# Kernel optimization log

Hardware: AMD Instinct MI355X
Metric: run time of the kernel (lower is better)

## Reference

```python
import jax, jax.numpy as jnp
import numpy as np

NH, NOPE_D, ROPE_D, V_D, R = 16, 48, 16, 64, 128
EPS = 1e-6

def rms_norm(x, w):
    norm = jax.lax.rsqrt(jnp.mean(jnp.square(x), axis=-1, keepdims=True) + EPS)
    return x * norm * w

def apply_rope(x, cos, sin):
    # x: (..., rope_d); cos/sin broadcastable (..., rope_d//2)
    d = x.shape[-1]
    x1, x2 = x[..., : d // 2], x[..., d // 2 :]
    return jnp.concatenate([x1 * cos - x2 * sin, x2 * cos + x1 * sin], axis=-1)

def setup_inputs() -> dict:
    key = jax.random.key(0)
    ks = jax.random.split(key, 8)
    B, T, D = 2, 2048, 1024
    s = lambda fan_in: 1.0 / np.sqrt(fan_in)
    return {
        "x": jax.random.normal(ks[0], (B, T, D), jnp.float32),
        "cos": jax.random.uniform(ks[1], (T, ROPE_D // 2), jnp.float32),
        "sin": jax.random.uniform(ks[2], (T, ROPE_D // 2), jnp.float32),
        "Wq": jax.random.normal(ks[3], (NH * (NOPE_D + ROPE_D), D), jnp.float32) * s(D),
        "q_norm_w": jnp.ones((NOPE_D + ROPE_D,), jnp.float32),
        "Wkva": jax.random.normal(ks[4], (R + ROPE_D, D), jnp.float32) * s(D),
        "kva_norm_w": jnp.ones((R,), jnp.float32),
        "Wkvb": jax.random.normal(ks[5], (NH * (NOPE_D + V_D), R), jnp.float32) * s(R),
        "Wo": jax.random.normal(ks[6], (D, NH * V_D), jnp.float32) * s(NH * V_D),
    }

def reference(x, cos, sin, Wq, q_norm_w, Wkva, kva_norm_w, Wkvb, Wo):
    B, T, D = x.shape
    # Q path: project, per-head RMSNorm over (nope+rope) dims, split
    q = (x @ Wq.T).reshape(B, T, NH, NOPE_D + ROPE_D)
    q = rms_norm(q, q_norm_w)
    q_nope, q_rope = q[..., :NOPE_D], q[..., NOPE_D:]
    # Low-rank KV path
    kv_a = x @ Wkva.T  # (B,T,R+ROPE_D)
    kv_latent = rms_norm(kv_a[..., :R], kva_norm_w)
    k_rope_raw = kv_a[..., R:]  # (B,T,ROPE_D) shared across heads
    kv_b = (kv_latent @ Wkvb.T).reshape(B, T, NH, NOPE_D + V_D)
    k_nope, v = kv_b[..., :NOPE_D], kv_b[..., NOPE_D:]
    # Decoupled RoPE
    cos_t = cos[None, :T, None, :]  # (1,T,1,rope_d/2)
    sin_t = sin[None, :T, None, :]
    q_rope = apply_rope(q_rope, cos_t, sin_t)
    k_rope = apply_rope(k_rope_raw[:, :, None, :], cos[None, :T, None, :], sin[None, :T, None, :])
    k_rope = jnp.broadcast_to(k_rope, (B, T, NH, ROPE_D))
    q_full = jnp.concatenate([q_nope, q_rope], axis=-1)  # (B,T,NH,64)
    k_full = jnp.concatenate([k_nope, k_rope], axis=-1)
    # Causal attention, scale = 1/sqrt(nope+rope)
    scale = (NOPE_D + ROPE_D) ** -0.5
    scores = jnp.einsum("bqhd,bkhd->bhqk", q_full, k_full) * scale
    causal = jnp.tril(jnp.ones((T, T), bool))
    scores = jnp.where(causal[None, None], scores, -jnp.inf)
    attn = jax.nn.softmax(scores, axis=-1)
    out = jnp.einsum("bhqk,bkhd->bqhd", attn, v).reshape(B, T, NH * V_D)
    return out @ Wo.T
```

## Files before the change

kernel.cpp:

```cpp
#include <hip/hip_runtime.h>
#include <hip/hip_bf16.h>
#include <math.h>

#define NH 16
#define T_ 2048
#define B_ 2
#define D_ 1024
#define EPS 1e-6f

typedef __attribute__((ext_vector_type(8))) short bf16x8;
typedef __attribute__((ext_vector_type(4))) short bf16x4;
typedef __attribute__((ext_vector_type(4))) float f32x4;

__device__ __forceinline__ unsigned pack_bf16(float a, float b){
  __hip_bfloat162 t = __float22bfloat162_rn(make_float2(a, b));
  unsigned r; __builtin_memcpy(&r, &t, 4); return r;
}

__device__ __forceinline__ void gload_lds16(const void* g, void* l){
  __builtin_amdgcn_global_load_lds((const __attribute__((address_space(1))) void*)g,
                                   (__attribute__((address_space(3))) void*)l, 16, 0, 0);
}

__device__ __forceinline__ f32x4 mfma16(bf16x4 a, bf16x4 b, f32x4 c){
#if __has_builtin(__builtin_amdgcn_mfma_f32_16x16x16bf16_1k)
  return __builtin_amdgcn_mfma_f32_16x16x16bf16_1k(a, b, c, 0, 0, 0);
#else
  asm volatile("v_mfma_f32_16x16x16_bf16 %0, %1, %2, %0" : "+v"(c) : "v"(a), "v"(b));
  return c;
#endif
}

__global__ __launch_bounds__(256)
void cvt5(const float* __restrict__ x, const float* __restrict__ wq,
          const float* __restrict__ wkva, const float* __restrict__ wkvb,
          const float* __restrict__ wo,
          __hip_bfloat16* __restrict__ xb, __hip_bfloat16* __restrict__ wqb,
          __hip_bfloat16* __restrict__ wkvab, __hip_bfloat16* __restrict__ wkvbb,
          __hip_bfloat16* __restrict__ wob)
{
  const int i = blockIdx.x * 256 + threadIdx.x;
  const float* s; __hip_bfloat16* d; size_t soff, doff;
  if      (i < 1048576) { s = x;    d = xb;    soff = doff = i; }
  else if (i < 1310720) { s = wq;   d = wqb;   soff = doff = i - 1048576; }
  else if (i < 1347584) { s = wkva; d = wkvab; soff = doff = i - 1310720; }
  else if (i < 1404928) {
    const int off = i - 1347584;
    const int srow = off >> 5, c4 = off & 31;
    const int h = srow / 112, dd = srow % 112;
    const int drow = (dd < 48) ? (h*48 + dd) : (768 + h*64 + (dd - 48));
    s = wkvb; d = wkvbb; soff = off; doff = (size_t)drow*32 + c4;
  }
  else                  { s = wo;   d = wob;   soff = doff = i - 1404928; }
  float4 v = *(const float4*)(s + soff * 4);
  *(__hip_bfloat162*)(d + doff * 4)     = __float22bfloat162_rn(make_float2(v.x, v.y));
  *(__hip_bfloat162*)(d + doff * 4 + 2) = __float22bfloat162_rn(make_float2(v.z, v.w));
}

template<typename CT>
__global__ __launch_bounds__(256, 2)
void gemm_bt64(const __hip_bfloat16* __restrict__ A, const __hip_bfloat16* __restrict__ W,
               CT* __restrict__ C, int M, int N, int K)
{
  __shared__ __hip_bfloat16 As[2][128 * 64];
  __shared__ __hip_bfloat16 Ws[2][64 * 64];
  const int tid = threadIdx.x;
  const int wv = tid >> 6, lane = tid & 63;
  const int m = lane & 15, quad = lane >> 4;
  const int bm = blockIdx.y * 128, bn = blockIdx.x * 64;

  const __hip_bfloat16* ga[4];
  const __hip_bfloat16* gw[2];
  #pragma unroll
  for (int i = 0; i < 4; i++) {
    const int slot = i*256 + tid;
    const int row = slot >> 3, cb = slot & 7;
    ga[i] = A + (size_t)(bm + row) * K + ((cb ^ (row & 7)) << 3);
  }
  #pragma unroll
  for (int i = 0; i < 2; i++) {
    const int slot = i*256 + tid;
    const int row = slot >> 3, cb = slot & 7;
    int wr = bn + row; if (wr >= N) wr = N - 1;
    gw[i] = W + (size_t)wr * K + ((cb ^ (row & 7)) << 3);
  }
  auto stage = [&](int buf){
    #pragma unroll
    for (int i = 0; i < 4; i++) { gload_lds16(ga[i], &As[buf][(i*256 + wv*64)*8]); ga[i] += 64; }
    #pragma unroll
    for (int i = 0; i < 2; i++) { gload_lds16(gw[i], &Ws[buf][(i*256 + wv*64)*8]); gw[i] += 64; }
  };

  f32x4 acc[2][4];
  #pragma unroll
  for (int mi = 0; mi < 2; mi++)
    #pragma unroll
    for (int nj = 0; nj < 4; nj++) acc[mi][nj] = (f32x4){0.f,0.f,0.f,0.f};

  stage(0);
  const int iters = K >> 6;
  for (int it = 0; it < iters; it++) {
    const int cur = it & 1;
    __syncthreads();
    if (it + 1 < iters) stage(cur ^ 1);
    #pragma unroll
    for (int ks = 0; ks < 2; ks++) {
      const int cb = ((ks*4 + quad) ^ (m & 7)) << 3;
      bf16x8 af[2], wf[4];
      #pragma unroll
      for (int mi = 0; mi < 2; mi++)
        af[mi] = *(const bf16x8*)(&As[cur][(wv*32 + mi*16 + m) * 64 + cb]);
      #pragma unroll
      for (int nj = 0; nj < 4; nj++)
        wf[nj] = *(const bf16x8*)(&Ws[cur][(nj*16 + m) * 64 + cb]);
      #pragma unroll
      for (int mi = 0; mi < 2; mi++)
        #pragma unroll
        for (int nj = 0; nj < 4; nj++)
          acc[mi][nj] = __builtin_amdgcn_mfma_f32_16x16x32_bf16(af[mi], wf[nj], acc[mi][nj], 0, 0, 0);
    }
  }

  #pragma unroll
  for (int mi = 0; mi < 2; mi++)
    #pragma unroll
    for (int nj = 0; nj < 4; nj++) {
      const int col = bn + nj*16 + m;
      if (col < N) {
        #pragma unroll
        for (int r = 0; r < 4; r++) {
          const int row = bm + wv*32 + mi*16 + quad*4 + r;
          if constexpr (sizeof(CT) == 2)
            C[(size_t)row * N + col] = (CT)__float2bfloat16(acc[mi][nj][r]);
          else
            C[(size_t)row * N + col] = acc[mi][nj][r];
        }
      }
    }
}

__global__ __launch_bounds__(256, 2)
void gemm_qkva(const __hip_bfloat16* __restrict__ A, const __hip_bfloat16* __restrict__ Wqb,
               const __hip_bfloat16* __restrict__ Wkvab,
               const float* __restrict__ qw, const float* __restrict__ kw,
               const float* __restrict__ cosp, const float* __restrict__ sinp,
               __hip_bfloat16* __restrict__ qb, __hip_bfloat16* __restrict__ kvl16,
               __hip_bfloat16* __restrict__ krope16)
{
  __shared__ __hip_bfloat16 As[2][128 * 64];
  __shared__ __hip_bfloat16 Ws[2][128 * 64];
  const int K = 1024;
  const int tid = threadIdx.x;
  const int wv = tid >> 6, lane = tid & 63;
  const int m = lane & 15, quad = lane >> 4;
  const int wr = wv >> 1, wc = wv & 1;
  const int bm = blockIdx.y * 128;
  const bool isq = blockIdx.x < 8;
  const __hip_bfloat16* W = isq ? Wqb : Wkvab;
  const int bn = isq ? blockIdx.x*128 : (blockIdx.x - 8)*128;
  const int Nw = isq ? 1024 : 144;

  const __hip_bfloat16* ga[4];
  const __hip_bfloat16* gw[4];
  #pragma unroll
  for (int i = 0; i < 4; i++) {
    const int slot = i*256 + tid;
    const int row = slot >> 3, cb = slot & 7;
    ga[i] = A + (size_t)(bm + row) * K + ((cb ^ (row & 7)) << 3);
    int wrow = bn + row; if (wrow >= Nw) wrow = Nw - 1;
    gw[i] = W + (size_t)wrow * K + ((cb ^ (row & 7)) << 3);
  }
  auto stage = [&](int buf){
    #pragma unroll
    for (int i = 0; i < 4; i++) { gload_lds16(ga[i], &As[buf][(i*256 + wv*64)*8]); ga[i] += 64; }
    #pragma unroll
    for (int i = 0; i < 4; i++) { gload_lds16(gw[i], &Ws[buf][(i*256 + wv*64)*8]); gw[i] += 64; }
  };

  f32x4 acc[4][4];
  #pragma unroll
  for (int mi = 0; mi < 4; mi++)
    #pragma unroll
    for (int nj = 0; nj < 4; nj++) acc[mi][nj] = (f32x4){0.f,0.f,0.f,0.f};

  stage(0);
  for (int it = 0; it < 16; it++) {
    const int cur = it & 1;
    __syncthreads();
    if (it < 15) stage(cur ^ 1);
    #pragma unroll
    for (int ks = 0; ks < 2; ks++) {
      const int cb = ((ks*4 + quad) ^ (m & 7)) << 3;
      bf16x8 af[4], wf[4];
      #pragma unroll
      for (int mi = 0; mi < 4; mi++)
        af[mi] = *(const bf16x8*)(&As[cur][(wr*64 + mi*16 + m) * 64 + cb]);
      #pragma unroll
      for (int nj = 0; nj < 4; nj++)
        wf[nj] = *(const bf16x8*)(&Ws[cur][(wc*64 + nj*16 + m) * 64 + cb]);
      #pragma unroll
      for (int mi = 0; mi < 4; mi++)
        #pragma unroll
        for (int nj = 0; nj < 4; nj++)
          acc[mi][nj] = __builtin_amdgcn_mfma_f32_16x16x32_bf16(af[mi], wf[nj], acc[mi][nj], 0, 0, 0);
    }
  }

  if (isq) {
    const int head = blockIdx.x*2 + wc;
    float qwv[4];
    #pragma unroll
    for (int nj = 0; nj < 4; nj++) qwv[nj] = qw[nj*16 + m];
    const int j = m & 7;
    const float qscale = 0.125f * 1.44269504f;
    #pragma unroll
    for (int mi = 0; mi < 4; mi++) {
      #pragma unroll
      for (int r = 0; r < 4; r++) {
        float ss = 0.f;
        #pragma unroll
        for (int nj = 0; nj < 4; nj++) { const float t = acc[mi][nj][r]; ss = fmaf(t, t, ss); }
        ss += __shfl_xor(ss, 1, 64); ss += __shfl_xor(ss, 2, 64);
        ss += __shfl_xor(ss, 4, 64); ss += __shfl_xor(ss, 8, 64);
        const float nrm = rsqrtf(ss * (1.0f/64.0f) + EPS);
        float v[4];
        #pragma unroll
        for (int nj = 0; nj < 4; nj++) v[nj] = acc[mi][nj][r] * nrm * qwv[nj];
        const int grow = bm + wr*64 + mi*16 + quad*4 + r;
        const int t = grow & (T_ - 1);
        const int b = grow >> 11;
        const float part = __shfl_xor(v[3], 8, 64);
        const float c = cosp[t*8 + j], sn = sinp[t*8 + j];
        v[3] = (m < 8) ? (v[3]*c - part*sn) : (v[3]*c + part*sn);
        __hip_bfloat16* dst = qb + ((size_t)(b*NH + head)*T_ + t)*64 + m;
        #pragma unroll
        for (int nj = 0; nj < 4; nj++) dst[nj*16] = __float2bfloat16(v[nj] * qscale);
      }
    }
  } else if (bn == 0) {
    __syncthreads();
    float* P = (float*)As;
    float part[4][4];
    #pragma unroll
    for (int mi = 0; mi < 4; mi++)
      #pragma unroll
      for (int r = 0; r < 4; r++) {
        float ss = 0.f;
        #pragma unroll
        for (int nj = 0; nj < 4; nj++) { const float t = acc[mi][nj][r]; ss = fmaf(t, t, ss); }
        ss += __shfl_xor(ss, 1, 64); ss += __shfl_xor(ss, 2, 64);
        ss += __shfl_xor(ss, 4, 64); ss += __shfl_xor(ss, 8, 64);
        part[mi][r] = ss;
        if (m == 0) P[((wc*2 + wr)*4 + mi)*16 + quad*4 + r] = ss;
      }
    __syncthreads();
    float kwv[4];
    #pragma unroll
    for (int nj = 0; nj < 4; nj++) kwv[nj] = kw[wc*64 + nj*16 + m];
    #pragma unroll
    for (int mi = 0; mi < 4; mi++)
      #pragma unroll
      for (int r = 0; r < 4; r++) {
        const float tot = part[mi][r] + P[(((wc^1)*2 + wr)*4 + mi)*16 + quad*4 + r];
        const float nrm = rsqrtf(tot * (1.0f/128.0f) + EPS);
        const int row = bm + wr*64 + mi*16 + quad*4 + r;
        #pragma unroll
        for (int nj = 0; nj < 4; nj++)
          kvl16[(size_t)row*128 + wc*64 + nj*16 + m]
              = __float2bfloat16(acc[mi][nj][r] * nrm * kwv[nj]);
      }
  } else {
    if (wc == 0) {
      const int j = m & 7;
      #pragma unroll
      for (int mi = 0; mi < 4; mi++)
        #pragma unroll
        for (int r = 0; r < 4; r++) {
          const int row = bm + wr*64 + mi*16 + quad*4 + r;
          const int t = row & (T_ - 1);
          const float v = acc[mi][0][r];
          const float part = __shfl_xor(v, 8, 64);
          const float c = cosp[t*8 + j], sn = sinp[t*8 + j];
          krope16[(size_t)row*16 + m] = __float2bfloat16((m < 8) ? (v*c - part*sn)
                                                                 : (v*c + part*sn));
        }
    }
  }
}

__global__ __launch_bounds__(256, 2)
void gemm_kvb(const __hip_bfloat16* __restrict__ A, const __hip_bfloat16* __restrict__ W,
              __hip_bfloat16* __restrict__ knope, __hip_bfloat16* __restrict__ vt)
{
  __shared__ __hip_bfloat16 As[2][128 * 64];
  __shared__ __hip_bfloat16 Ws[2][64 * 64];
  const int K = 128;
  const int tid = threadIdx.x;
  const int wv = tid >> 6, lane = tid & 63;
  const int m = lane & 15, quad = lane >> 4;
  const int bm = blockIdx.y * 128, bn = blockIdx.x * 64;

  const __hip_bfloat16* ga[4];
  const __hip_bfloat16* gw[2];
  #pragma unroll
  for (int i = 0; i < 4; i++) {
    const int slot = i*256 + tid;
    const int row = slot >> 3, cb = slot & 7;
    ga[i] = A + (size_t)(bm + row) * K + ((cb ^ (row & 7)) << 3);
  }
  #pragma unroll
  for (int i = 0; i < 2; i++) {
    const int slot = i*256 + tid;
    const int row = slot >> 3, cb = slot & 7;
    gw[i] = W + (size_t)(bn + row) * K + ((cb ^ (row & 7)) << 3);
  }
  auto stage = [&](int buf){
    #pragma unroll
    for (int i = 0; i < 4; i++) { gload_lds16(ga[i], &As[buf][(i*256 + wv*64)*8]); ga[i] += 64; }
    #pragma unroll
    for (int i = 0; i < 2; i++) { gload_lds16(gw[i], &Ws[buf][(i*256 + wv*64)*8]); gw[i] += 64; }
  };

  f32x4 acc[2][4];
  #pragma unroll
  for (int mi = 0; mi < 2; mi++)
    #pragma unroll
    for (int nj = 0; nj < 4; nj++) acc[mi][nj] = (f32x4){0.f,0.f,0.f,0.f};

  stage(0);
  for (int it = 0; it < 2; it++) {
    const int cur = it & 1;
    __syncthreads();
    if (it == 0) stage(1);
    #pragma unroll
    for (int ks = 0; ks < 2; ks++) {
      const int cb = ((ks*4 + quad) ^ (m & 7)) << 3;
      bf16x8 af[2], wf[4];
      #pragma unroll
      for (int mi = 0; mi < 2; mi++)
        af[mi] = *(const bf16x8*)(&As[cur][(wv*32 + mi*16 + m) * 64 + cb]);
      #pragma unroll
      for (int nj = 0; nj < 4; nj++)
        wf[nj] = *(const bf16x8*)(&Ws[cur][(nj*16 + m) * 64 + cb]);
      #pragma unroll
      for (int mi = 0; mi < 2; mi++)
        #pragma unroll
        for (int nj = 0; nj < 4; nj++)
          acc[mi][nj] = __builtin_amdgcn_mfma_f32_16x16x32_bf16(af[mi], wf[nj], acc[mi][nj], 0, 0, 0);
    }
  }

  if (bn < 768) {
    #pragma unroll
    for (int mi = 0; mi < 2; mi++)
      #pragma unroll
      for (int nj = 0; nj < 4; nj++) {
        const int col = bn + nj*16 + m;
        #pragma unroll
        for (int r = 0; r < 4; r++) {
          const int row = bm + wv*32 + mi*16 + quad*4 + r;
          knope[(size_t)row * 768 + col] = __float2bfloat16(acc[mi][nj][r]);
        }
      }
  } else {
    __syncthreads();
    short* TL = (short*)&As[0][0];
    #pragma unroll
    for (int mi = 0; mi < 2; mi++)
      #pragma unroll
      for (int nj = 0; nj < 4; nj++) {
        const int d = nj*16 + m;
        #pragma unroll
        for (int r = 0; r < 4; r++) {
          const int tl = wv*32 + mi*16 + quad*4 + r;
          __hip_bfloat16 hv = __float2bfloat16(acc[mi][nj][r]);
          short sv; __builtin_memcpy(&sv, &hv, 2);
          TL[d*136 + tl] = sv;
        }
      }
    __syncthreads();
    const int h = (bn - 768) >> 6;
    const int b = bm >> 11;
    const int t0 = bm & (T_ - 1);
    #pragma unroll
    for (int i = 0; i < 4; i++) {
      const int unit = i*256 + tid;
      const int d = unit >> 4, tu = unit & 15;
      *(bf16x8*)(vt + ((size_t)(b*NH + h)*64 + d)*T_ + t0 + tu*8)
          = *(const bf16x8*)(TL + d*136 + tu*8);
    }
  }
}

__global__ __launch_bounds__(256, 4)
void attn_tile(const __hip_bfloat16* __restrict__ qb,
               const __hip_bfloat16* __restrict__ knope,
               const __hip_bfloat16* __restrict__ krope16,
               const __hip_bfloat16* __restrict__ vt16,
               __hip_bfloat16* __restrict__ aout)
{
  __shared__ __hip_bfloat16 SL[16384];
  const int tid = threadIdx.x;
  const int wv = tid >> 6, lane = tid & 63;
  const int m = lane & 15, quad = lane >> 4;
  const int wq = wv >> 1, wk = wv & 1;
  const int idx = (blockIdx.x + blockIdx.y) & 31;
  const int pj = idx & 7, pk = idx >> 3;
  const int qt = (pk == 0) ? pj : (pk == 1) ? (15 - pj) : (pk == 2) ? (16 + pj) : (31 - pj);
  const int bh = blockIdx.y;
  const int b = bh >> 4, h = bh & 15;
  const int nt = qt + 1;

  bf16x8 q0[2], q1[2];
  #pragma unroll
  for (int t2 = 0; t2 < 2; t2++) {
    const __hip_bfloat16* qr = qb + ((size_t)bh*T_ + qt*64 + wq*32 + t2*16 + m)*64 + quad*8;
    q0[t2] = *(const bf16x8*)qr; q1[t2] = *(const bf16x8*)(qr + 32);
  }

  const __hip_bfloat16* pK[2]; size_t iK[2];
  const __hip_bfloat16* pV[2];
  #pragma unroll
  for (int i = 0; i < 2; i++) {
    const int slot = i*256 + tid;
    const int krow = slot >> 3;
    const int kde = (slot & 7) ^ (krow & 7);
    if (kde < 6) { pK[i] = knope + (size_t)(b*T_ + krow)*768 + h*48 + kde*8; iK[i] = (size_t)64*768; }
    else         { pK[i] = krope16 + (size_t)(b*T_ + krow)*16 + (kde-6)*8;   iK[i] = (size_t)64*16; }
    pV[i] = vt16 + ((size_t)bh*64 + krow)*T_ + kde*8;
  }

  auto stage = [&](int buf){
    #pragma unroll
    for (int i = 0; i < 2; i++) {
      gload_lds16(pK[i], SL + buf*4096 + (i*256 + wv*64)*8);
      gload_lds16(pV[i], SL + 8192 + buf*4096 + (i*256 + wv*64)*8);
      pK[i] += iK[i]; pV[i] += 64;
    }
  };

  f32x4 o[2][4];
  #pragma unroll
  for (int t2 = 0; t2 < 2; t2++)
    #pragma unroll
    for (int vs = 0; vs < 4; vs++) o[t2][vs] = (f32x4){0.f,0.f,0.f,0.f};
  float lrun[2] = {0.f, 0.f};

  const int swk = quad ^ (m & 7);
  const int qh = quad >> 1, ql = quad & 1;
  stage(0);

  for (int kt = 0; kt < nt; kt++) {
    const int cur = kt & 1;
    __syncthreads();
    if (kt + 1 < nt) stage(cur ^ 1);
    const __hip_bfloat16* Kc = SL + cur*4096;
    const __hip_bfloat16* Vc = SL + 8192 + cur*4096;
    const bool dtile = (kt == qt);

    f32x4 s[2][2];
    __builtin_amdgcn_s_setprio(1);
    #pragma unroll
    for (int ks = 0; ks < 2; ks++) {
      const int gk2 = 2*wk + ks;
      if (!dtile || gk2 <= 2*wq + 1) {
        const __hip_bfloat16* kr = Kc + (wk*32 + ks*16 + m)*64;
        const bf16x8 kf0 = *(const bf16x8*)(kr + swk*8);
        const bf16x8 kf1 = *(const bf16x8*)(kr + (swk^4)*8);
        #pragma unroll
        for (int t2 = 0; t2 < 2; t2++) {
          if (!dtile || gk2 <= 2*wq + t2) {
            f32x4 z = (f32x4){0.f,0.f,0.f,0.f};
            z = __builtin_amdgcn_mfma_f32_16x16x32_bf16(kf0, q0[t2], z, 0, 0, 0);
            z = __builtin_amdgcn_mfma_f32_16x16x32_bf16(kf1, q1[t2], z, 0, 0, 0);
            s[t2][ks] = z;
          } else {
            s[t2][ks] = (f32x4){-1e30f,-1e30f,-1e30f,-1e30f};
          }
        }
      } else {
        s[0][ks] = (f32x4){-1e30f,-1e30f,-1e30f,-1e30f};
        s[1][ks] = (f32x4){-1e30f,-1e30f,-1e30f,-1e30f};
      }
    }
    __builtin_amdgcn_s_setprio(0);

    if (dtile) {
      #pragma unroll
      for (int ks = 0; ks < 2; ks++)
        #pragma unroll
        for (int t2 = 0; t2 < 2; t2++)
          if (2*wk + ks == 2*wq + t2) {
            #pragma unroll
            for (int r = 0; r < 4; r++)
              if (quad*4 + r > m) s[t2][ks][r] = -1e30f;
          }
    }

    bf16x4 u[2][2];
    #pragma unroll
    for (int t2 = 0; t2 < 2; t2++)
      #pragma unroll
      for (int ks = 0; ks < 2; ks++) {
        float p0 = exp2f(s[t2][ks][0] - 48.0f), p1 = exp2f(s[t2][ks][1] - 48.0f);
        float p2 = exp2f(s[t2][ks][2] - 48.0f), p3 = exp2f(s[t2][ks][3] - 48.0f);
        lrun[t2] += (p0 + p1) + (p2 + p3);
        union { unsigned ui[2]; bf16x4 v; } uu;
        uu.ui[0] = pack_bf16(p0, p1);
        uu.ui[1] = pack_bf16(p2, p3);
        u[t2][ks] = uu.v;
      }

    __builtin_amdgcn_s_setprio(1);
    #pragma unroll
    for (int vs = 0; vs < 4; vs++) {
      #pragma unroll
      for (int ks = 0; ks < 2; ks++) {
        const int gk2 = 2*wk + ks;
        if (!dtile || gk2 <= 2*wq + 1) {
          const bf16x4 vf = *(const bf16x4*)(Vc + (vs*16 + m)*64
                              + (((wk*4 + ks*2 + qh) ^ (m & 7)) << 3) + (ql << 2));
          #pragma unroll
          for (int t2 = 0; t2 < 2; t2++)
            if (!dtile || gk2 <= 2*wq + t2)
              o[t2][vs] = mfma16(vf, u[t2][ks], o[t2][vs]);
        }
      }
    }
    __builtin_amdgcn_s_setprio(0);
  }

  __syncthreads();
  float* FB = (float*)SL;
  float* LB = ((float*)SL) + 4096;
  if (wk == 1) {
    #pragma unroll
    for (int t2 = 0; t2 < 2; t2++)
      #pragma unroll
      for (int vs = 0; vs < 4; vs++)
        #pragma unroll
        for (int r = 0; r < 4; r++)
          FB[wq*2048 + ((t2*4 + vs)*4 + r)*64 + lane] = o[t2][vs][r];
    LB[wq*128 + lane]      = lrun[0];
    LB[wq*128 + 64 + lane] = lrun[1];
  }
  __syncthreads();
  if (wk == 0) {
    #pragma unroll
    for (int t2 = 0; t2 < 2; t2++)
      #pragma unroll
      for (int vs = 0; vs < 4; vs++)
        #pragma unroll
        for (int r = 0; r < 4; r++)
          o[t2][vs][r] += FB[wq*2048 + ((t2*4 + vs)*4 + r)*64 + lane];
    lrun[0] += LB[wq*128 + lane];
    lrun[1] += LB[wq*128 + 64 + lane];
    #pragma unroll
    for (int t2 = 0; t2 < 2; t2++) {
      float l = lrun[t2];
      l += __shfl_xor(l, 16, 64);
      l += __shfl_xor(l, 32, 64);
      const float inv = 1.0f / l;
      const size_t base = (size_t)(b*T_ + qt*64 + wq*32 + t2*16 + m) * 1024 + h*64 + quad*4;
      #pragma unroll
      for (int vs = 0; vs < 4; vs++) {
        union { unsigned ui[2]; bf16x4 v; } pkv;
        pkv.ui[0] = pack_bf16(o[t2][vs][0] * inv, o[t2][vs][1] * inv);
        pkv.ui[1] = pack_bf16(o[t2][vs][2] * inv, o[t2][vs][3] * inv);
        *(bf16x4*)(aout + base + vs*16) = pkv.v;
      }
    }
  }
}

extern "C" void kernel_launch(void* const* d_in, const int* in_sizes, int n_in,
                              void* d_out, int out_size, void* d_ws, size_t ws_size,
                              hipStream_t stream)
{
  const float* x    = (const float*)d_in[0];
  const float* cosp = (const float*)d_in[1];
  const float* sinp = (const float*)d_in[2];
  const float* Wq   = (const float*)d_in[3];
  const float* qw   = (const float*)d_in[4];
  const float* Wkva = (const float*)d_in[5];
  const float* kw   = (const float*)d_in[6];
  const float* Wkvb = (const float*)d_in[7];
  const float* Wo   = (const float*)d_in[8];
  float* out = (float*)d_out;

  float* kva = (float*)d_ws;
  __hip_bfloat16* xb16    = (__hip_bfloat16*)(kva + 589824);
  __hip_bfloat16* knope16 = xb16 + 4194304;
  __hip_bfloat16* kvl16   = knope16 + 3145728;
  __hip_bfloat16* qb16    = kvl16 + 524288;
  __hip_bfloat16* vt16    = qb16 + 4194304;
  __hip_bfloat16* krope16 = vt16 + 4194304;
  __hip_bfloat16* Wqb     = krope16 + 65536;
  __hip_bfloat16* Wkvab   = Wqb + 1048576;
  __hip_bfloat16* Wkvbb   = Wkvab + 147456;
  __hip_bfloat16* Wob     = Wkvbb + 229376;
  __hip_bfloat16* ab16    = Wob + 1048576;

  const int M = B_ * T_;

  cvt5<<<6512, 256, 0, stream>>>(x, Wq, Wkva, Wkvb, Wo, xb16, Wqb, Wkvab, Wkvbb, Wob);
  gemm_qkva<<<dim3(10, 32), 256, 0, stream>>>(xb16, Wqb, Wkvab, qw, kw, cosp, sinp,
                                              qb16, kvl16, krope16);
  gemm_kvb<<<dim3(28, 32), 256, 0, stream>>>(kvl16, Wkvbb, knope16, vt16);
  attn_tile<<<dim3(32, B_ * NH), 256, 0, stream>>>(qb16, knope16, krope16, vt16, ab16);
  gemm_bt64<float><<<dim3(16, 32), 256, 0, stream>>>(ab16, Wob, out, M, 1024, 1024);
}
```

Before: 178.0 us.

## Split long causal query tiles across blocks and merge partials via atomic counter

Reassigns causal attention work so that each block handles a roughly equal number of key tiles. The longest query tiles (24-31) are split into two key-range halves run by different blocks. Each half writes unnormalised partial outputs and row sums to workspace scratch and bumps an atomic counter; the second block to finish merges both halves and writes the output. The counters are zeroed in the conversion kernel. This trades extra scratch traffic and a global atomic handshake for a shorter critical path than the previous uneven per-block tile counts.

```diff
diff --git a/kernel.cpp b/kernel.cpp
--- a/kernel.cpp
+++ b/kernel.cpp
@@ -37,8 +37,9 @@
           const float* __restrict__ wo,
           __hip_bfloat16* __restrict__ xb, __hip_bfloat16* __restrict__ wqb,
           __hip_bfloat16* __restrict__ wkvab, __hip_bfloat16* __restrict__ wkvbb,
-          __hip_bfloat16* __restrict__ wob)
+          __hip_bfloat16* __restrict__ wob, int* __restrict__ ctr)
 {
+  if (blockIdx.x == 0) ctr[threadIdx.x] = 0;
   const int i = blockIdx.x * 256 + threadIdx.x;
   const float* s; __hip_bfloat16* d; size_t soff, doff;
   if      (i < 1048576) { s = x;    d = xb;    soff = doff = i; }
@@ -397,177 +398,245 @@
                const __hip_bfloat16* __restrict__ knope,
                const __hip_bfloat16* __restrict__ krope16,
                const __hip_bfloat16* __restrict__ vt16,
-               __hip_bfloat16* __restrict__ aout)
+               __hip_bfloat16* __restrict__ aout,
+               float* __restrict__ scr, int* __restrict__ ctr)
 {
   __shared__ __hip_bfloat16 SL[16384];
+  __shared__ int flagv;
   const int tid = threadIdx.x;
   const int wv = tid >> 6, lane = tid & 63;
   const int m = lane & 15, quad = lane >> 4;
   const int wq = wv >> 1, wk = wv & 1;
-  const int idx = (blockIdx.x + blockIdx.y) & 31;
-  const int pj = idx & 7, pk = idx >> 3;
-  const int qt = (pk == 0) ? pj : (pk == 1) ? (15 - pj) : (pk == 2) ? (16 + pj) : (31 - pj);
   const int bh = blockIdx.y;
   const int b = bh >> 4, h = bh & 15;
-  const int nt = qt + 1;
-
-  bf16x8 q0[2], q1[2];
-  #pragma unroll
-  for (int t2 = 0; t2 < 2; t2++) {
-    const __hip_bfloat16* qr = qb + ((size_t)bh*T_ + qt*64 + wq*32 + t2*16 + m)*64 + quad*8;
-    q0[t2] = *(const bf16x8*)qr; q1[t2] = *(const bf16x8*)(qr + 32);
-  }
-
-  const __hip_bfloat16* pK[2]; size_t iK[2];
-  const __hip_bfloat16* pV[2];
-  #pragma unroll
-  for (int i = 0; i < 2; i++) {
-    const int slot = i*256 + tid;
-    const int krow = slot >> 3;
-    const int kde = (slot & 7) ^ (krow & 7);
-    if (kde < 6) { pK[i] = knope + (size_t)(b*T_ + krow)*768 + h*48 + kde*8; iK[i] = (size_t)64*768; }
-    else         { pK[i] = krope16 + (size_t)(b*T_ + krow)*16 + (kde-6)*8;   iK[i] = (size_t)64*16; }
-    pV[i] = vt16 + ((size_t)bh*64 + krow)*T_ + kde*8;
-  }
-
-  auto stage = [&](int buf){
-    #pragma unroll
-    for (int i = 0; i < 2; i++) {
-      gload_lds16(pK[i], SL + buf*4096 + (i*256 + wv*64)*8);
-      gload_lds16(pV[i], SL + 8192 + buf*4096 + (i*256 + wv*64)*8);
-      pK[i] += iK[i]; pV[i] += 64;
-    }
-  };
-
-  f32x4 o[2][4];
-  #pragma unroll
-  for (int t2 = 0; t2 < 2; t2++)
-    #pragma unroll
-    for (int vs = 0; vs < 4; vs++) o[t2][vs] = (f32x4){0.f,0.f,0.f,0.f};
-  float lrun[2] = {0.f, 0.f};
+
+  const int idx = (blockIdx.x + blockIdx.y) & 31;
+  const int i = idx & 7, p = idx >> 3;
+  int nseg = 1, sQt[2], sK0[2], sNk[2], sMd[2];
+  if (i < 7) {
+    if      (p == 0) { sQt[0]=23-i; sK0[0]=0;  sNk[0]=24-i; sMd[0]=0; }
+    else if (p == 1) { sQt[0]=24+i; sK0[0]=0;  sNk[0]=16;   sMd[0]=1; }
+    else if (p == 2) { sQt[0]=8+i;  sK0[0]=0;  sNk[0]=9+i;  sMd[0]=0; }
+    else { nseg=2; sQt[0]=i;    sK0[0]=0;  sNk[0]=i+1;  sMd[0]=0;
+                   sQt[1]=31-i; sK0[1]=16; sNk[1]=16-i; sMd[1]=2; }
+  } else {
+    if      (p == 0) { sQt[0]=15; sK0[0]=0;  sNk[0]=16; sMd[0]=0; }
+    else if (p == 1) { sQt[0]=16; sK0[0]=0;  sNk[0]=17; sMd[0]=0; }
+    else if (p == 2) { nseg=2; sQt[0]=7;  sK0[0]=0;  sNk[0]=8; sMd[0]=0;
+                               sQt[1]=24; sK0[1]=16; sNk[1]=9; sMd[1]=2; }
+    else             { sQt[0]=31; sK0[0]=0;  sNk[0]=16; sMd[0]=1; }
+  }
 
   const int swk = quad ^ (m & 7);
   const int qh = quad >> 1, ql = quad & 1;
-  stage(0);
-
-  for (int kt = 0; kt < nt; kt++) {
-    const int cur = kt & 1;
-    __syncthreads();
-    if (kt + 1 < nt) stage(cur ^ 1);
-    const __hip_bfloat16* Kc = SL + cur*4096;
-    const __hip_bfloat16* Vc = SL + 8192 + cur*4096;
-    const bool dtile = (kt == qt);
-
-    f32x4 s[2][2];
-    __builtin_amdgcn_s_setprio(1);
-    #pragma unroll
-    for (int ks = 0; ks < 2; ks++) {
-      const int gk2 = 2*wk + ks;
-      if (!dtile || gk2 <= 2*wq + 1) {
-        const __hip_bfloat16* kr = Kc + (wk*32 + ks*16 + m)*64;
-        const bf16x8 kf0 = *(const bf16x8*)(kr + swk*8);
-        const bf16x8 kf1 = *(const bf16x8*)(kr + (swk^4)*8);
-        #pragma unroll
-        for (int t2 = 0; t2 < 2; t2++) {
-          if (!dtile || gk2 <= 2*wq + t2) {
-            f32x4 z = (f32x4){0.f,0.f,0.f,0.f};
-            z = __builtin_amdgcn_mfma_f32_16x16x32_bf16(kf0, q0[t2], z, 0, 0, 0);
-            z = __builtin_amdgcn_mfma_f32_16x16x32_bf16(kf1, q1[t2], z, 0, 0, 0);
-            s[t2][ks] = z;
-          } else {
-            s[t2][ks] = (f32x4){-1e30f,-1e30f,-1e30f,-1e30f};
-          }
-        }
-      } else {
-        s[0][ks] = (f32x4){-1e30f,-1e30f,-1e30f,-1e30f};
-        s[1][ks] = (f32x4){-1e30f,-1e30f,-1e30f,-1e30f};
-      }
-    }
-    __builtin_amdgcn_s_setprio(0);
-
-    if (dtile) {
-      #pragma unroll
-      for (int ks = 0; ks < 2; ks++)
-        #pragma unroll
-        for (int t2 = 0; t2 < 2; t2++)
-          if (2*wk + ks == 2*wq + t2) {
-            #pragma unroll
-            for (int r = 0; r < 4; r++)
-              if (quad*4 + r > m) s[t2][ks][r] = -1e30f;
-          }
-    }
-
-    bf16x4 u[2][2];
+
+  for (int sg = 0; sg < nseg; sg++) {
+    const int qt = sQt[sg], k0 = sK0[sg], nk = sNk[sg], md = sMd[sg];
+
+    bf16x8 q0[2], q1[2];
+    #pragma unroll
+    for (int t2 = 0; t2 < 2; t2++) {
+      const __hip_bfloat16* qr = qb + ((size_t)bh*T_ + qt*64 + wq*32 + t2*16 + m)*64 + quad*8;
+      q0[t2] = *(const bf16x8*)qr; q1[t2] = *(const bf16x8*)(qr + 32);
+    }
+
+    const __hip_bfloat16* pK[2]; size_t iK[2];
+    const __hip_bfloat16* pV[2];
+    #pragma unroll
+    for (int ii = 0; ii < 2; ii++) {
+      const int slot = ii*256 + tid;
+      const int krow = slot >> 3;
+      const int kde = (slot & 7) ^ (krow & 7);
+      if (kde < 6) { pK[ii] = knope + (size_t)(b*T_ + k0*64 + krow)*768 + h*48 + kde*8; iK[ii] = (size_t)64*768; }
+      else         { pK[ii] = krope16 + (size_t)(b*T_ + k0*64 + krow)*16 + (kde-6)*8;   iK[ii] = (size_t)64*16; }
+      pV[ii] = vt16 + ((size_t)bh*64 + krow)*T_ + k0*64 + kde*8;
+    }
+    auto stage = [&](int buf){
+      #pragma unroll
+      for (int ii = 0; ii < 2; ii++) {
+        gload_lds16(pK[ii], SL + buf*4096 + (ii*256 + wv*64)*8);
+        gload_lds16(pV[ii], SL + 8192 + buf*4096 + (ii*256 + wv*64)*8);
+        pK[ii] += iK[ii]; pV[ii] += 64;
+      }
+    };
+
+    f32x4 o[2][4];
     #pragma unroll
     for (int t2 = 0; t2 < 2; t2++)
       #pragma unroll
-      for (int ks = 0; ks < 2; ks++) {
-        float p0 = exp2f(s[t2][ks][0] - 48.0f), p1 = exp2f(s[t2][ks][1] - 48.0f);
-        float p2 = exp2f(s[t2][ks][2] - 48.0f), p3 = exp2f(s[t2][ks][3] - 48.0f);
-        lrun[t2] += (p0 + p1) + (p2 + p3);
-        union { unsigned ui[2]; bf16x4 v; } uu;
-        uu.ui[0] = pack_bf16(p0, p1);
-        uu.ui[1] = pack_bf16(p2, p3);
-        u[t2][ks] = uu.v;
-      }
-
-    __builtin_amdgcn_s_setprio(1);
-    #pragma unroll
-    for (int vs = 0; vs < 4; vs++) {
+      for (int vs = 0; vs < 4; vs++) o[t2][vs] = (f32x4){0.f,0.f,0.f,0.f};
+    float lrun[2] = {0.f, 0.f};
+
+    __syncthreads();
+    stage(0);
+
+    for (int k2 = 0; k2 < nk; k2++) {
+      const int kt = k0 + k2;
+      const int cur = k2 & 1;
+      __syncthreads();
+      if (k2 + 1 < nk) stage(cur ^ 1);
+      const __hip_bfloat16* Kc = SL + cur*4096;
+      const __hip_bfloat16* Vc = SL + 8192 + cur*4096;
+      const bool dtile = (kt == qt);
+
+      f32x4 s[2][2];
+      __builtin_amdgcn_s_setprio(1);
       #pragma unroll
       for (int ks = 0; ks < 2; ks++) {
         const int gk2 = 2*wk + ks;
         if (!dtile || gk2 <= 2*wq + 1) {
-          const bf16x4 vf = *(const bf16x4*)(Vc + (vs*16 + m)*64
-                              + (((wk*4 + ks*2 + qh) ^ (m & 7)) << 3) + (ql << 2));
+          const __hip_bfloat16* kr = Kc + (wk*32 + ks*16 + m)*64;
+          const bf16x8 kf0 = *(const bf16x8*)(kr + swk*8);
+          const bf16x8 kf1 = *(const bf16x8*)(kr + (swk^4)*8);
+          #pragma unroll
+          for (int t2 = 0; t2 < 2; t2++) {
+            if (!dtile || gk2 <= 2*wq + t2) {
+              f32x4 z = (f32x4){0.f,0.f,0.f,0.f};
+              z = __builtin_amdgcn_mfma_f32_16x16x32_bf16(kf0, q0[t2], z, 0, 0, 0);
+              z = __builtin_amdgcn_mfma_f32_16x16x32_bf16(kf1, q1[t2], z, 0, 0, 0);
+              s[t2][ks] = z;
+            } else {
+              s[t2][ks] = (f32x4){-1e30f,-1e30f,-1e30f,-1e30f};
+            }
+          }
+        } else {
+          s[0][ks] = (f32x4){-1e30f,-1e30f,-1e30f,-1e30f};
+          s[1][ks] = (f32x4){-1e30f,-1e30f,-1e30f,-1e30f};
+        }
+      }
+      __builtin_amdgcn_s_setprio(0);
+
+      if (dtile) {
+        #pragma unroll
+        for (int ks = 0; ks < 2; ks++)
           #pragma unroll
           for (int t2 = 0; t2 < 2; t2++)
-            if (!dtile || gk2 <= 2*wq + t2)
-              o[t2][vs] = mfma16(vf, u[t2][ks], o[t2][vs]);
-        }
-      }
-    }
-    __builtin_amdgcn_s_setprio(0);
-  }
-
-  __syncthreads();
-  float* FB = (float*)SL;
-  float* LB = ((float*)SL) + 4096;
-  if (wk == 1) {
-    #pragma unroll
-    for (int t2 = 0; t2 < 2; t2++)
-      #pragma unroll
-      for (int vs = 0; vs < 4; vs++)
-        #pragma unroll
-        for (int r = 0; r < 4; r++)
-          FB[wq*2048 + ((t2*4 + vs)*4 + r)*64 + lane] = o[t2][vs][r];
-    LB[wq*128 + lane]      = lrun[0];
-    LB[wq*128 + 64 + lane] = lrun[1];
-  }
-  __syncthreads();
-  if (wk == 0) {
-    #pragma unroll
-    for (int t2 = 0; t2 < 2; t2++)
-      #pragma unroll
-      for (int vs = 0; vs < 4; vs++)
-        #pragma unroll
-        for (int r = 0; r < 4; r++)
-          o[t2][vs][r] += FB[wq*2048 + ((t2*4 + vs)*4 + r)*64 + lane];
-    lrun[0] += LB[wq*128 + lane];
-    lrun[1] += LB[wq*128 + 64 + lane];
-    #pragma unroll
-    for (int t2 = 0; t2 < 2; t2++) {
-      float l = lrun[t2];
-      l += __shfl_xor(l, 16, 64);
-      l += __shfl_xor(l, 32, 64);
-      const float inv = 1.0f / l;
-      const size_t base = (size_t)(b*T_ + qt*64 + wq*32 + t2*16 + m) * 1024 + h*64 + quad*4;
+            if (2*wk + ks == 2*wq + t2) {
+              #pragma unroll
+              for (int r = 0; r < 4; r++)
+                if (quad*4 + r > m) s[t2][ks][r] = -1e30f;
+            }
+      }
+
+      bf16x4 u[2][2];
+      #pragma unroll
+      for (int t2 = 0; t2 < 2; t2++)
+        #pragma unroll
+        for (int ks = 0; ks < 2; ks++) {
+          float p0 = exp2f(s[t2][ks][0] - 48.0f), p1 = exp2f(s[t2][ks][1] - 48.0f);
+          float p2 = exp2f(s[t2][ks][2] - 48.0f), p3 = exp2f(s[t2][ks][3] - 48.0f);
+          lrun[t2] += (p0 + p1) + (p2 + p3);
+          union { unsigned ui[2]; bf16x4 v; } uu;
+          uu.ui[0] = pack_bf16(p0, p1);
+          uu.ui[1] = pack_bf16(p2, p3);
+          u[t2][ks] = uu.v;
+        }
+
+      __builtin_amdgcn_s_setprio(1);
       #pragma unroll
       for (int vs = 0; vs < 4; vs++) {
-        union { unsigned ui[2]; bf16x4 v; } pkv;
-        pkv.ui[0] = pack_bf16(o[t2][vs][0] * inv, o[t2][vs][1] * inv);
-        pkv.ui[1] = pack_bf16(o[t2][vs][2] * inv, o[t2][vs][3] * inv);
-        *(bf16x4*)(aout + base + vs*16) = pkv.v;
+        #pragma unroll
+        for (int ks = 0; ks < 2; ks++) {
+          const int gk2 = 2*wk + ks;
+          if (!dtile || gk2 <= 2*wq + 1) {
+            const bf16x4 vf = *(const bf16x4*)(Vc + (vs*16 + m)*64
+                                + (((wk*4 + ks*2 + qh) ^ (m & 7)) << 3) + (ql << 2));
+            #pragma unroll
+            for (int t2 = 0; t2 < 2; t2++)
+              if (!dtile || gk2 <= 2*wq + t2)
+                o[t2][vs] = mfma16(vf, u[t2][ks], o[t2][vs]);
+          }
+        }
+      }
+      __builtin_amdgcn_s_setprio(0);
+    }
+
+    __syncthreads();
+    float* FB = (float*)SL;
+    float* LB = ((float*)SL) + 4096;
+    if (wk == 1) {
+      #pragma unroll
+      for (int t2 = 0; t2 < 2; t2++)
+        #pragma unroll
+        for (int vs = 0; vs < 4; vs++)
+          #pragma unroll
+          for (int r = 0; r < 4; r++)
+            FB[wq*2048 + ((t2*4 + vs)*4 + r)*64 + lane] = o[t2][vs][r];
+      LB[wq*128 + lane]      = lrun[0];
+      LB[wq*128 + 64 + lane] = lrun[1];
+    }
+    __syncthreads();
+    if (wk == 0) {
+      #pragma unroll
+      for (int t2 = 0; t2 < 2; t2++)
+        #pragma unroll
+        for (int vs = 0; vs < 4; vs++)
+          #pragma unroll
+          for (int r = 0; r < 4; r++)
+            o[t2][vs][r] += FB[wq*2048 + ((t2*4 + vs)*4 + r)*64 + lane];
+      lrun[0] += LB[wq*128 + lane];
+      lrun[1] += LB[wq*128 + 64 + lane];
+      #pragma unroll
+      for (int t2 = 0; t2 < 2; t2++) {
+        lrun[t2] += __shfl_xor(lrun[t2], 16, 64);
+        lrun[t2] += __shfl_xor(lrun[t2], 32, 64);
+      }
+    }
+
+    if (md == 0) {
+      if (wk == 0) {
+        #pragma unroll
+        for (int t2 = 0; t2 < 2; t2++) {
+          const float inv = 1.0f / lrun[t2];
+          const size_t base = (size_t)(b*T_ + qt*64 + wq*32 + t2*16 + m) * 1024 + h*64 + quad*4;
+          #pragma unroll
+          for (int vs = 0; vs < 4; vs++) {
+            union { unsigned ui[2]; bf16x4 v; } pkv;
+            pkv.ui[0] = pack_bf16(o[t2][vs][0] * inv, o[t2][vs][1] * inv);
+            pkv.ui[1] = pack_bf16(o[t2][vs][2] * inv, o[t2][vs][3] * inv);
+            *(bf16x4*)(aout + base + vs*16) = pkv.v;
+          }
+        }
+      }
+    } else {
+      const int pair = (qt - 24)*32 + bh;
+      const int slot = md - 1;
+      float* sbase = scr + (size_t)(pair*2 + slot)*4160;
+      if (wk == 0) {
+        #pragma unroll
+        for (int t2 = 0; t2 < 2; t2++) {
+          const int q = wq*32 + t2*16 + m;
+          #pragma unroll
+          for (int vs = 0; vs < 4; vs++)
+            *(f32x4*)(sbase + q*64 + vs*16 + quad*4) = o[t2][vs];
+          if (quad == 0) sbase[4096 + q] = lrun[t2];
+        }
+      }
+      __syncthreads();
+      if (tid == 0) {
+        __threadfence();
+        flagv = __hip_atomic_fetch_add(&ctr[pair], 1, __ATOMIC_ACQ_REL,
+                                       __HIP_MEMORY_SCOPE_AGENT);
+      }
+      __syncthreads();
+      if (flagv == 1 && wk == 0) {
+        __threadfence();
+        const float* pb = scr + (size_t)(pair*2 + (slot^1))*4160;
+        #pragma unroll
+        for (int t2 = 0; t2 < 2; t2++) {
+          const int q = wq*32 + t2*16 + m;
+          const float lp = pb[4096 + q];
+          const float inv = 1.0f / (lrun[t2] + lp);
+          const size_t base = (size_t)(b*T_ + qt*64 + q) * 1024 + h*64 + quad*4;
+          #pragma unroll
+          for (int vs = 0; vs < 4; vs++) {
+            const f32x4 po = *(const f32x4*)(pb + q*64 + vs*16 + quad*4);
+            union { unsigned ui[2]; bf16x4 v; } pkv;
+            pkv.ui[0] = pack_bf16((o[t2][vs][0] + po[0]) * inv, (o[t2][vs][1] + po[1]) * inv);
+            pkv.ui[1] = pack_bf16((o[t2][vs][2] + po[2]) * inv, (o[t2][vs][3] + po[3]) * inv);
+            *(bf16x4*)(aout + base + vs*16) = pkv.v;
+          }
+        }
       }
     }
   }
@@ -588,6 +657,8 @@
   const float* Wo   = (const float*)d_in[8];
   float* out = (float*)d_out;
 
+  int*   actr = (int*)d_ws;
+  float* ascr = (float*)d_ws + 256;
   float* kva = (float*)d_ws;
   __hip_bfloat16* xb16    = (__hip_bfloat16*)(kva + 589824);
   __hip_bfloat16* knope16 = xb16 + 4194304;
@@ -603,10 +674,11 @@
 
   const int M = B_ * T_;
 
-  cvt5<<<6512, 256, 0, stream>>>(x, Wq, Wkva, Wkvb, Wo, xb16, Wqb, Wkvab, Wkvbb, Wob);
+  cvt5<<<6512, 256, 0, stream>>>(x, Wq, Wkva, Wkvb, Wo, xb16, Wqb, Wkvab, Wkvbb, Wob, actr);
   gemm_qkva<<<dim3(10, 32), 256, 0, stream>>>(xb16, Wqb, Wkvab, qw, kw, cosp, sinp,
                                               qb16, kvl16, krope16);
   gemm_kvb<<<dim3(28, 32), 256, 0, stream>>>(kvl16, Wkvbb, knope16, vt16);
-  attn_tile<<<dim3(32, B_ * NH), 256, 0, stream>>>(qb16, knope16, krope16, vt16, ab16);
+  attn_tile<<<dim3(32, B_ * NH), 256, 0, stream>>>(qb16, knope16, krope16, vt16, ab16,
+                                                   ascr, actr);
   gemm_bt64<float><<<dim3(16, 32), 256, 0, stream>>>(ab16, Wob, out, M, 1024, 1024);
 }
```

New measurement: 234.7 us. 1.32x slower.
